# Kernel optimization log

Measured on AMD Instinct MI355X. Metric: run time of the kernel, lower is better.

The kernel has to match this reference:

```python
import jax, jax.numpy as jnp
import numpy as np

D = 1024
H = 16
HD = D // H
MLP = 4 * D
EPS = 1e-5


def layernorm(x, g, b):
    mu = jnp.mean(x, axis=-1, keepdims=True)
    var = jnp.mean(jnp.square(x - mu), axis=-1, keepdims=True)
    return (x - mu) * jax.lax.rsqrt(var + EPS) * g + b


def setup_inputs() -> dict:
    key = jax.random.key(0)
    ks = jax.random.split(key, 12)
    s = 0.02
    return {
        "x": jax.random.normal(ks[0], (2, 2048, D), jnp.float32),
        "ln1_g": jnp.ones((D,), jnp.float32),
        "ln1_b": jnp.zeros((D,), jnp.float32),
        "lnm_g": jnp.ones((D,), jnp.float32),
        "lnm_b": jnp.zeros((D,), jnp.float32),
        "qkv_w": jax.random.normal(ks[1], (D, 3 * D), jnp.float32) * s,
        "qkv_b": jnp.zeros((3 * D,), jnp.float32),
        "proj_w": jax.random.normal(ks[2], (D, D), jnp.float32) * s,
        "proj_b": jnp.zeros((D,), jnp.float32),
        "fc1_w": jax.random.normal(ks[3], (D, MLP), jnp.float32) * s,
        "fc1_b": jnp.zeros((MLP,), jnp.float32),
        "fc2_w": jax.random.normal(ks[4], (MLP, D), jnp.float32) * s,
        "fc2_b": jnp.zeros((D,), jnp.float32),
    }


def reference(x, ln1_g, ln1_b, lnm_g, lnm_b, qkv_w, qkv_b, proj_w, proj_b,
              fc1_w, fc1_b, fc2_w, fc2_b):
    B, N, _ = x.shape
    scale = HD ** -0.5
    # --- self-attention on norm1(x) ---
    h = layernorm(x, ln1_g, ln1_b)
    qkv = h @ qkv_w + qkv_b                       # [B, N, 3D]
    qkv = qkv.reshape(B, N, 3, H, HD)
    q, k, v = qkv[:, :, 0], qkv[:, :, 1], qkv[:, :, 2]  # [B, N, H, HD]
    attn = jnp.einsum("bqhd,bkhd->bhqk", q, k) * scale
    attn = jax.nn.softmax(attn, axis=-1)
    o = jnp.einsum("bhqk,bkhd->bqhd", attn, v).reshape(B, N, D)
    x = x + (o @ proj_w + proj_b)
    # --- MLP ---
    m = layernorm(x, lnm_g, lnm_b)
    m = jax.nn.gelu(m @ fc1_w + fc1_b, approximate=False)
    x = x + (m @ fc2_w + fc2_b)
    return x
```

## Files before the change

kernel.cpp:

```cpp
#include <hip/hip_runtime.h>

typedef __bf16 bf16_t;
typedef bf16_t bf16x4 __attribute__((ext_vector_type(4)));
typedef bf16_t bf16x8 __attribute__((ext_vector_type(8)));
typedef float f32x4 __attribute__((ext_vector_type(4)));
typedef unsigned short u16x8 __attribute__((ext_vector_type(8)));

#define MFMA(a, b, c) __builtin_amdgcn_mfma_f32_16x16x32_bf16(a, b, c, 0, 0, 0)

__device__ inline float exp2_fast(float x) {
  float r;
  asm volatile("v_exp_f32 %0, %1" : "=v"(r) : "v"(x));
  return r;
}

__device__ inline void gll16(const bf16_t* g, bf16_t* l) {
  __builtin_amdgcn_global_load_lds(
      (const __attribute__((address_space(1))) unsigned int*)(g),
      (__attribute__((address_space(3))) unsigned int*)(l), 16, 0, 0);
}

__device__ inline float gelu_f(float v) {
  float ax = fabsf(v) * 0.70710678118f;
  float t = __builtin_amdgcn_rcpf(1.0f + 0.3275911f * ax);
  float p = ((((1.061405429f * t - 1.453152027f) * t + 1.421413741f) * t -
              0.284496736f) * t + 0.254829592f) * t;
  float e = exp2_fast(-ax * ax * 1.4426950408889634f);
  float erf = 1.0f - p * e;
  erf = v < 0.f ? -erf : erf;
  return 0.5f * v * (1.0f + erf);
}

__global__ __launch_bounds__(256) void ln_kernel(const float* __restrict__ x,
                                                 const float* __restrict__ g,
                                                 const float* __restrict__ b,
                                                 bf16_t* __restrict__ out) {
  long row = blockIdx.x;
  const float4* xr = (const float4*)(x + row * 1024);
  float4 v = xr[threadIdx.x];
  float s = v.x + v.y + v.z + v.w;
  float s2 = v.x * v.x + v.y * v.y + v.z * v.z + v.w * v.w;
#pragma unroll
  for (int m = 32; m >= 1; m >>= 1) {
    s += __shfl_xor(s, m);
    s2 += __shfl_xor(s2, m);
  }
  __shared__ float red[8];
  int wid = threadIdx.x >> 6;
  if ((threadIdx.x & 63) == 0) {
    red[wid] = s;
    red[4 + wid] = s2;
  }
  __syncthreads();
  s = red[0] + red[1] + red[2] + red[3];
  s2 = red[4] + red[5] + red[6] + red[7];
  float mu = s * (1.f / 1024.f);
  float rs = rsqrtf(s2 * (1.f / 1024.f) - mu * mu + 1e-5f);
  float4 gv = ((const float4*)g)[threadIdx.x];
  float4 bv = ((const float4*)b)[threadIdx.x];
  bf16_t o0 = (bf16_t)((v.x - mu) * rs * gv.x + bv.x);
  bf16_t o1 = (bf16_t)((v.y - mu) * rs * gv.y + bv.y);
  bf16_t o2 = (bf16_t)((v.z - mu) * rs * gv.z + bv.z);
  bf16_t o3 = (bf16_t)((v.w - mu) * rs * gv.w + bv.w);
  ushort4 pk;
  pk.x = *(unsigned short*)&o0;
  pk.y = *(unsigned short*)&o1;
  pk.z = *(unsigned short*)&o2;
  pk.w = *(unsigned short*)&o3;
  *(ushort4*)(out + row * 1024 + threadIdx.x * 4) = pk;
}

__global__ __launch_bounds__(256) void wconv_all(
    const float* __restrict__ qkv_w, bf16_t* __restrict__ qkv_wt,
    const float* __restrict__ proj_w, bf16_t* __restrict__ proj_wt,
    const float* __restrict__ fc1_w, bf16_t* __restrict__ fc1_wt,
    const float* __restrict__ fc2_w, bf16_t* __restrict__ fc2_wt) {
  int id = blockIdx.x;
  const float* W;
  bf16_t* Wt;
  int K, N, bx, by;
  if (id < 768) {
    W = qkv_w; Wt = qkv_wt; K = 1024; N = 3072; bx = id % 48; by = id / 48;
  } else if (id < 1024) {
    int l = id - 768;
    W = proj_w; Wt = proj_wt; K = 1024; N = 1024; bx = l % 16; by = l / 16;
  } else if (id < 2048) {
    int l = id - 1024;
    W = fc1_w; Wt = fc1_wt; K = 1024; N = 4096; bx = l % 64; by = l / 64;
  } else {
    int l = id - 2048;
    W = fc2_w; Wt = fc2_wt; K = 4096; N = 1024; bx = l % 16; by = l / 16;
  }
  __shared__ float t[64][65];
  int n0 = bx * 64, k0 = by * 64;
  int tid = threadIdx.x;
  int c4 = tid & 15;
  int r = tid >> 4;
#pragma unroll
  for (int s = 0; s < 4; s++) {
    int k = r + s * 16;
    float4 v = *(const float4*)(W + (long)(k0 + k) * N + n0 + c4 * 4);
    t[k][c4 * 4] = v.x;
    t[k][c4 * 4 + 1] = v.y;
    t[k][c4 * 4 + 2] = v.z;
    t[k][c4 * 4 + 3] = v.w;
  }
  __syncthreads();
  int n = tid >> 2;
  int kc = (tid & 3) * 16;
  ushort4 pk[4];
#pragma unroll
  for (int c = 0; c < 4; c++) {
#pragma unroll
    for (int j = 0; j < 4; j++) {
      bf16_t x = (bf16_t)t[kc + c * 4 + j][n];
      ((unsigned short*)&pk[c])[j] = *(unsigned short*)&x;
    }
  }
  bf16_t* dst = Wt + (long)(n0 + n) * K + k0 + kc;
#pragma unroll
  for (int c = 0; c < 4; c++) *(ushort4*)(dst + c * 4) = pk[c];
}

#define STAGE_PTR(DA, DB, k0)                 \
  gll16(ga + (k0), DA + w * 512);             \
  gll16(ga + (k0) + astep, DA + 4096 + w * 512); \
  gll16(gb + (k0), DB + w * 512);

#define COMPUTE(LA, LB)                                                \
  {                                                                    \
    bf16x8 af[4], bfr[4];                                              \
    _Pragma("unroll") for (int mt = 0; mt < 4; mt++) af[mt] =          \
        *(const bf16x8*)(LA + (wm + mt * 16 + l15) * 32 + quad * 8);   \
    _Pragma("unroll") for (int nt = 0; nt < 4; nt++) bfr[nt] =         \
        *(const bf16x8*)(LB + (wn + nt * 16 + l15) * 32 + quad * 8);   \
    _Pragma("unroll") for (int mt = 0; mt < 4; mt++)                   \
        _Pragma("unroll") for (int nt = 0; nt < 4; nt++) acc[mt][nt] = \
            MFMA(af[mt], bfr[nt], acc[mt][nt]);                        \
  }

#define WB3 asm volatile("s_waitcnt vmcnt(3)\ns_barrier" ::: "memory")
#define WB0 asm volatile("s_waitcnt vmcnt(0)\ns_barrier" ::: "memory")

__global__ __launch_bounds__(512, 4) void gemm_kernel(
    const bf16_t* __restrict__ A, const bf16_t* __restrict__ Bt,
    const float* __restrict__ bias, const float* __restrict__ resid,
    void* __restrict__ Cout, int M, int N, int K, int epi) {
  __shared__ bf16_t lA0[256 * 32], lB0[128 * 32];
  __shared__ bf16_t lA1[256 * 32], lB1[128 * 32];
  __shared__ bf16_t lA2[256 * 32], lB2[128 * 32];
  int tid = threadIdx.x;
  int bn = blockIdx.x, bm = blockIdx.y;
  int kchunk = K / gridDim.z;
  int kbeg = blockIdx.z * kchunk, kend = kbeg + kchunk;

  int lane = tid & 63, w = tid >> 6;
  int quad = lane >> 4, l15 = lane & 15;
  int wm = (w & 3) * 64, wn = (w >> 2) * 64;

  f32x4 acc[4][4];
#pragma unroll
  for (int i = 0; i < 4; i++)
#pragma unroll
    for (int j = 0; j < 4; j++) acc[i][j] = (f32x4){0.f, 0.f, 0.f, 0.f};

  const bf16_t* ga = A + (long)(bm * 256 + w * 16 + (lane >> 2)) * K + (lane & 3) * 8;
  const bf16_t* gb = Bt + (long)(bn * 128 + w * 16 + (lane >> 2)) * K + (lane & 3) * 8;
  long astep = (long)128 * K;

  int nit = (kend - kbeg) >> 5;
  bf16_t *A0 = lA0, *A1 = lA1, *A2 = lA2;
  bf16_t *B0 = lB0, *B1 = lB1, *B2 = lB2;
  STAGE_PTR(A0, B0, kbeg);
  STAGE_PTR(A1, B1, kbeg + 32);
  for (int i = 0; i < nit; i++) {
    if (i + 1 < nit) { WB3; } else { WB0; }
    if (i + 2 < nit) {
      int ks = kbeg + (i + 2) * 32;
      STAGE_PTR(A2, B2, ks);
    }
    COMPUTE(A0, B0);
    bf16_t* t;
    t = A0; A0 = A1; A1 = A2; A2 = t;
    t = B0; B0 = B1; B1 = B2; B2 = t;
  }

#pragma unroll
  for (int mt = 0; mt < 4; mt++) {
#pragma unroll
    for (int r = 0; r < 4; r++) {
      long row = bm * 256 + wm + mt * 16 + quad * 4 + r;
#pragma unroll
      for (int nt = 0; nt < 4; nt++) {
        int col = bn * 128 + wn + nt * 16 + l15;
        long idx = row * N + col;
        if (epi == 3) {
          ((bf16_t*)Cout)[(long)blockIdx.z * M * N + idx] = (bf16_t)acc[mt][nt][r];
        } else {
          float v = acc[mt][nt][r] + bias[col];
          if (epi == 1) {
            ((float*)Cout)[idx] = v + resid[idx];
          } else if (epi == 2) {
            ((bf16_t*)Cout)[idx] = (bf16_t)gelu_f(v);
          } else {
            ((bf16_t*)Cout)[idx] = (bf16_t)v;
          }
        }
      }
    }
  }
}

__global__ __launch_bounds__(256) void reduce_ln_kernel(
    const bf16_t* __restrict__ p, const float* __restrict__ bias,
    const float* __restrict__ resid, float* __restrict__ x1,
    const float* __restrict__ g, const float* __restrict__ bb,
    bf16_t* __restrict__ mb) {
  const long MN = (long)4096 * 1024;
  long row = blockIdx.x;
  int t = threadIdx.x;
  bf16x4 a0 = *(const bf16x4*)(p + row * 1024 + t * 4);
  bf16x4 a1 = *(const bf16x4*)(p + MN + row * 1024 + t * 4);
  bf16x4 a2 = *(const bf16x4*)(p + 2 * MN + row * 1024 + t * 4);
  bf16x4 a3 = *(const bf16x4*)(p + 3 * MN + row * 1024 + t * 4);
  float4 r = ((const float4*)(resid + row * 1024))[t];
  float4 bv = ((const float4*)bias)[t];
  float4 v;
  v.x = (float)a0[0] + (float)a1[0] + (float)a2[0] + (float)a3[0] + r.x + bv.x;
  v.y = (float)a0[1] + (float)a1[1] + (float)a2[1] + (float)a3[1] + r.y + bv.y;
  v.z = (float)a0[2] + (float)a1[2] + (float)a2[2] + (float)a3[2] + r.z + bv.z;
  v.w = (float)a0[3] + (float)a1[3] + (float)a2[3] + (float)a3[3] + r.w + bv.w;
  ((float4*)(x1 + row * 1024))[t] = v;
  float s = v.x + v.y + v.z + v.w;
  float s2 = v.x * v.x + v.y * v.y + v.z * v.z + v.w * v.w;
#pragma unroll
  for (int m = 32; m >= 1; m >>= 1) {
    s += __shfl_xor(s, m);
    s2 += __shfl_xor(s2, m);
  }
  __shared__ float red[8];
  int wid = t >> 6;
  if ((t & 63) == 0) {
    red[wid] = s;
    red[4 + wid] = s2;
  }
  __syncthreads();
  s = red[0] + red[1] + red[2] + red[3];
  s2 = red[4] + red[5] + red[6] + red[7];
  float mu = s * (1.f / 1024.f);
  float rs = rsqrtf(s2 * (1.f / 1024.f) - mu * mu + 1e-5f);
  float4 gv = ((const float4*)g)[t];
  float4 b2 = ((const float4*)bb)[t];
  bf16_t o0 = (bf16_t)((v.x - mu) * rs * gv.x + b2.x);
  bf16_t o1 = (bf16_t)((v.y - mu) * rs * gv.y + b2.y);
  bf16_t o2 = (bf16_t)((v.z - mu) * rs * gv.z + b2.z);
  bf16_t o3 = (bf16_t)((v.w - mu) * rs * gv.w + b2.w);
  ushort4 pk;
  pk.x = *(unsigned short*)&o0;
  pk.y = *(unsigned short*)&o1;
  pk.z = *(unsigned short*)&o2;
  pk.w = *(unsigned short*)&o3;
  *(ushort4*)(mb + row * 1024 + t * 4) = pk;
}

__global__ __launch_bounds__(256) void reduce4_kernel(const bf16_t* __restrict__ p,
                                                      const float* __restrict__ bias,
                                                      const float* __restrict__ resid,
                                                      float* __restrict__ out) {
  long i = (long)blockIdx.x * 256 + threadIdx.x;
  const long MN = (long)4096 * 1024;
  bf16x4 a0 = *(const bf16x4*)(p + i * 4);
  bf16x4 a1 = *(const bf16x4*)(p + MN + i * 4);
  bf16x4 a2 = *(const bf16x4*)(p + 2 * MN + i * 4);
  bf16x4 a3 = *(const bf16x4*)(p + 3 * MN + i * 4);
  float4 r = ((const float4*)resid)[i];
  float4 bv = ((const float4*)bias)[i & 255];
  float4 o;
  o.x = (float)a0[0] + (float)a1[0] + (float)a2[0] + (float)a3[0] + r.x + bv.x;
  o.y = (float)a0[1] + (float)a1[1] + (float)a2[1] + (float)a3[1] + r.y + bv.y;
  o.z = (float)a0[2] + (float)a1[2] + (float)a2[2] + (float)a3[2] + r.z + bv.z;
  o.w = (float)a0[3] + (float)a1[3] + (float)a2[3] + (float)a3[3] + r.w + bv.w;
  ((float4*)out)[i] = o;
}

#define LDV 72

__global__ __launch_bounds__(256) void attn_kernel(const bf16_t* __restrict__ qkv,
                                                   bf16_t* __restrict__ o) {
  const int LD = 3072;
  int id = blockIdx.x;
  int within = id >> 3;
  int bh = (id & 7) * 4 + (within >> 4);
  int qt = within & 15;
  int h = bh & 15, b = bh >> 4;

  int tid = threadIdx.x, w = tid >> 6, lane = tid & 63;
  int quad = lane >> 4, l15 = lane & 15;
  int qrow = qt * 128 + w * 32;
  const bf16_t* base = qkv + (long)b * 2048 * LD + h * 64;
  const bf16_t* Qp = base;
  const bf16_t* Kp = base + 1024;
  const bf16_t* Vp = base + 2048;

  __shared__ bf16_t lK[2][64 * 64];
  __shared__ bf16_t lV[2][64 * LDV];
  __shared__ bf16_t lP[4][32 * LDV];
  bf16_t* myp = lP[w];

  const bf16_t* kg =
      Kp + (long)(w * 16 + (lane >> 3)) * LD + (((lane & 7) ^ (lane >> 3)) & 7) * 8;
  int kk = tid & 31;
  int d0 = (tid >> 5) * 8;
  const bf16_t* vg = Vp + (long)(2 * kk) * LD + d0;

  gll16(kg, lK[0] + w * 1024);
  gll16(kg + 8 * (long)LD, lK[0] + w * 1024 + 512);
  u16x8 va = *(const u16x8*)(vg);
  u16x8 vb = *(const u16x8*)(vg + LD);

  bf16x8 qf[2][2];
#pragma unroll
  for (int qi = 0; qi < 2; qi++)
#pragma unroll
    for (int d = 0; d < 2; d++)
      qf[qi][d] =
          *(const bf16x8*)(Qp + (long)(qrow + qi * 16 + l15) * LD + d * 32 + quad * 8);

  f32x4 oacc[2][4];
#pragma unroll
  for (int qi = 0; qi < 2; qi++)
#pragma unroll
    for (int t = 0; t < 4; t++) oacc[qi][t] = (f32x4){0.f, 0.f, 0.f, 0.f};
  float li_p[2][4] = {{0.f, 0.f, 0.f, 0.f}, {0.f, 0.f, 0.f, 0.f}};
  const float c2 = 0.18033688011112042f;

  int sw0 = (quad ^ l15) & 7;
  int sw1 = ((quad + 4) ^ l15) & 7;

  for (int it = 0; it < 32; it++) {
    int cur = it & 1, nxt = cur ^ 1;
    asm volatile("s_waitcnt vmcnt(0)\ns_barrier" ::: "memory");
    unsigned int* lvw = (unsigned int*)lV[cur];
#pragma unroll
    for (int j = 0; j < 8; j++)
      lvw[(d0 + j) * (LDV / 2) + kk] = (unsigned int)va[j] | ((unsigned int)vb[j] << 16);
    u16x8 va_n = va, vb_n = vb;
    if (it + 1 < 32) {
      long koff2 = (long)(it + 1) * 64 * LD;
      gll16(kg + koff2, lK[nxt] + w * 1024);
      gll16(kg + koff2 + 8 * (long)LD, lK[nxt] + w * 1024 + 512);
      va_n = *(const u16x8*)(vg + koff2);
      vb_n = *(const u16x8*)(vg + koff2 + LD);
    }
    asm volatile("s_waitcnt lgkmcnt(0)\ns_barrier" ::: "memory");

    bf16x8 kf[4][2];
#pragma unroll
    for (int st = 0; st < 4; st++) {
      const bf16_t* krow = lK[cur] + (st * 16 + l15) * 64;
      kf[st][0] = *(const bf16x8*)(krow + sw0 * 8);
      kf[st][1] = *(const bf16x8*)(krow + sw1 * 8);
    }
    f32x4 s[2][4];
#pragma unroll
    for (int qi = 0; qi < 2; qi++)
#pragma unroll
      for (int st = 0; st < 4; st++) {
        f32x4 z = (f32x4){0.f, 0.f, 0.f, 0.f};
        z = MFMA(qf[qi][0], kf[st][0], z);
        s[qi][st] = MFMA(qf[qi][1], kf[st][1], z);
      }

#pragma unroll
    for (int qi = 0; qi < 2; qi++)
#pragma unroll
      for (int st = 0; st < 4; st++)
#pragma unroll
        for (int r = 0; r < 4; r++) {
          float p = exp2_fast(s[qi][st][r] * c2);
          s[qi][st][r] = p;
          li_p[qi][r] += p;
        }

#pragma unroll
    for (int qi = 0; qi < 2; qi++)
#pragma unroll
      for (int r = 0; r < 4; r++)
#pragma unroll
        for (int st = 0; st < 4; st++)
          myp[(qi * 16 + quad * 4 + r) * LDV + st * 16 + l15] = (bf16_t)s[qi][st][r];
    asm volatile("s_waitcnt lgkmcnt(0)" ::: "memory");

    bf16x8 pa[2][2];
#pragma unroll
    for (int qi = 0; qi < 2; qi++) {
      pa[qi][0] = *(const bf16x8*)(myp + (qi * 16 + l15) * LDV + quad * 8);
      pa[qi][1] = *(const bf16x8*)(myp + (qi * 16 + l15) * LDV + 32 + quad * 8);
    }
#pragma unroll
    for (int t = 0; t < 4; t++) {
      const bf16_t* vr = lV[cur] + (t * 16 + l15) * LDV + quad * 8;
      bf16x8 v0 = *(const bf16x8*)(vr);
      bf16x8 v1 = *(const bf16x8*)(vr + 32);
#pragma unroll
      for (int qi = 0; qi < 2; qi++) {
        oacc[qi][t] = MFMA(pa[qi][0], v0, oacc[qi][t]);
        oacc[qi][t] = MFMA(pa[qi][1], v1, oacc[qi][t]);
      }
    }
    va = va_n;
    vb = vb_n;
  }

#pragma unroll
  for (int qi = 0; qi < 2; qi++) {
    float li[4];
#pragma unroll
    for (int r = 0; r < 4; r++) {
      float s = li_p[qi][r];
#pragma unroll
      for (int x = 8; x >= 1; x >>= 1) s += __shfl_xor(s, x);
      li[r] = s;
    }
#pragma unroll
    for (int t = 0; t < 4; t++)
#pragma unroll
      for (int r = 0; r < 4; r++) {
        long q = qrow + qi * 16 + quad * 4 + r;
        o[((long)b * 2048 + q) * 1024 + h * 64 + t * 16 + l15] =
            (bf16_t)(oacc[qi][t][r] / li[r]);
      }
  }
}

extern "C" void kernel_launch(void* const* d_in, const int* in_sizes, int n_in,
                              void* d_out, int out_size, void* d_ws, size_t ws_size,
                              hipStream_t stream) {
  (void)in_sizes; (void)n_in; (void)out_size; (void)ws_size;
  const float* x = (const float*)d_in[0];
  const float* ln1_g = (const float*)d_in[1];
  const float* ln1_b = (const float*)d_in[2];
  const float* lnm_g = (const float*)d_in[3];
  const float* lnm_b = (const float*)d_in[4];
  const float* qkv_w = (const float*)d_in[5];
  const float* qkv_b = (const float*)d_in[6];
  const float* proj_w = (const float*)d_in[7];
  const float* proj_b = (const float*)d_in[8];
  const float* fc1_w = (const float*)d_in[9];
  const float* fc1_b = (const float*)d_in[10];
  const float* fc2_w = (const float*)d_in[11];
  const float* fc2_b = (const float*)d_in[12];
  float* out = (float*)d_out;

  const int M = 4096;
  const int D_ = 1024, MLP_ = 4096, QKV = 3072;

  char* ws = (char*)d_ws;
  bf16_t* h = (bf16_t*)(ws);
  bf16_t* qkvb = (bf16_t*)(ws + (8u << 20));
  bf16_t* ob = (bf16_t*)(ws + (32u << 20));
  float* x1 = (float*)(ws + (40u << 20));
  bf16_t* mb = (bf16_t*)(ws + (56u << 20));
  bf16_t* gb = (bf16_t*)(ws + (64u << 20));
  bf16_t* qkv_wt = (bf16_t*)(ws + (96u << 20));
  bf16_t* proj_wt = (bf16_t*)(ws + (102u << 20));
  bf16_t* fc1_wt = (bf16_t*)(ws + (104u << 20));
  bf16_t* fc2_wt = (bf16_t*)(ws + (112u << 20));
  bf16_t* p_proj = (bf16_t*)(ws);
  bf16_t* p_fc2 = (bf16_t*)(ws);

  wconv_all<<<3072, 256, 0, stream>>>(qkv_w, qkv_wt, proj_w, proj_wt, fc1_w, fc1_wt,
                                      fc2_w, fc2_wt);

  ln_kernel<<<M, 256, 0, stream>>>(x, ln1_g, ln1_b, h);
  gemm_kernel<<<dim3(QKV / 128, M / 256), 512, 0, stream>>>(h, qkv_wt, qkv_b, nullptr,
                                                            qkvb, M, QKV, D_, 0);
  attn_kernel<<<512, 256, 0, stream>>>(qkvb, ob);
  gemm_kernel<<<dim3(D_ / 128, M / 256, 4), 512, 0, stream>>>(ob, proj_wt, nullptr,
                                                              nullptr, p_proj, M, D_,
                                                              D_, 3);
  reduce_ln_kernel<<<M, 256, 0, stream>>>(p_proj, proj_b, x, x1, lnm_g, lnm_b, mb);
  gemm_kernel<<<dim3(MLP_ / 128, M / 256), 512, 0, stream>>>(mb, fc1_wt, fc1_b,
                                                             nullptr, gb, M, MLP_, D_,
                                                             2);
  gemm_kernel<<<dim3(D_ / 128, M / 256, 4), 512, 0, stream>>>(gb, fc2_wt, nullptr,
                                                              nullptr, p_fc2, M, D_,
                                                              MLP_, 3);
  reduce4_kernel<<<4096, 256, 0, stream>>>(p_fc2, fc2_b, x1, out);
}
```

Baseline: 390.9 us.

## Add 256x256-tile triple-buffered GEMM for fc1 and fold softmax scale into Q

Adds a new GEMM kernel with 256x256 output tiles, 8 waves and a three-stage global-to-LDS pipeline, used only for the fc1+GELU GEMM. Larger tiles raise arithmetic intensity per loaded byte, but the grid shrinks to 256 blocks and register pressure goes up. Separately, the attention kernel pre-multiplies Q by the exp2 softmax scale once, removing a per-score multiply in the inner loop. That adds a bf16 rounding of the scaled Q values.

```diff
diff --git a/kernel.cpp b/kernel.cpp
--- a/kernel.cpp
+++ b/kernel.cpp
@@ -206,6 +206,82 @@
             ((bf16_t*)Cout)[idx] = (bf16_t)v;
           }
         }
+      }
+    }
+  }
+}
+
+#define STAGE256(DA, DB, k0)                  \
+  gll16(ga + (k0), DA + w * 512);             \
+  gll16(ga + (k0) + astep, DA + 4096 + w * 512); \
+  gll16(gb + (k0), DB + w * 512);             \
+  gll16(gb + (k0) + astep, DB + 4096 + w * 512);
+
+__global__ __launch_bounds__(512, 2) void gemm256_kernel(
+    const bf16_t* __restrict__ A, const bf16_t* __restrict__ Bt,
+    const float* __restrict__ bias, void* __restrict__ Cout, int M, int N, int K) {
+  __shared__ bf16_t lA0[256 * 32], lB0[256 * 32];
+  __shared__ bf16_t lA1[256 * 32], lB1[256 * 32];
+  __shared__ bf16_t lA2[256 * 32], lB2[256 * 32];
+  int tid = threadIdx.x;
+  int bn = blockIdx.x, bm = blockIdx.y;
+  int lane = tid & 63, w = tid >> 6;
+  int quad = lane >> 4, l15 = lane & 15;
+  int wm = (w & 3) * 64, wn = (w >> 2) * 128;
+
+  f32x4 acc[4][8];
+#pragma unroll
+  for (int i = 0; i < 4; i++)
+#pragma unroll
+    for (int j = 0; j < 8; j++) acc[i][j] = (f32x4){0.f, 0.f, 0.f, 0.f};
+
+  const bf16_t* ga = A + (long)(bm * 256 + w * 16 + (lane >> 2)) * K + (lane & 3) * 8;
+  const bf16_t* gb = Bt + (long)(bn * 256 + w * 16 + (lane >> 2)) * K + (lane & 3) * 8;
+  long astep = (long)128 * K;
+
+  int nit = K >> 5;
+  bf16_t *A0 = lA0, *A1 = lA1, *A2 = lA2;
+  bf16_t *B0 = lB0, *B1 = lB1, *B2 = lB2;
+  STAGE256(A0, B0, 0);
+  STAGE256(A1, B1, 32);
+  for (int i = 0; i < nit; i++) {
+    if (i + 1 < nit) {
+      asm volatile("s_waitcnt vmcnt(4)\ns_barrier" ::: "memory");
+    } else {
+      asm volatile("s_waitcnt vmcnt(0)\ns_barrier" ::: "memory");
+    }
+    if (i + 2 < nit) {
+      int ks = (i + 2) * 32;
+      STAGE256(A2, B2, ks);
+    }
+    {
+      bf16x8 af[4], bfr[8];
+#pragma unroll
+      for (int mt = 0; mt < 4; mt++)
+        af[mt] = *(const bf16x8*)(A0 + (wm + mt * 16 + l15) * 32 + quad * 8);
+#pragma unroll
+      for (int nt = 0; nt < 8; nt++)
+        bfr[nt] = *(const bf16x8*)(B0 + (wn + nt * 16 + l15) * 32 + quad * 8);
+#pragma unroll
+      for (int mt = 0; mt < 4; mt++)
+#pragma unroll
+        for (int nt = 0; nt < 8; nt++) acc[mt][nt] = MFMA(af[mt], bfr[nt], acc[mt][nt]);
+    }
+    bf16_t* t;
+    t = A0; A0 = A1; A1 = A2; A2 = t;
+    t = B0; B0 = B1; B1 = B2; B2 = t;
+  }
+
+#pragma unroll
+  for (int mt = 0; mt < 4; mt++) {
+#pragma unroll
+    for (int r = 0; r < 4; r++) {
+      long row = bm * 256 + wm + mt * 16 + quad * 4 + r;
+#pragma unroll
+      for (int nt = 0; nt < 8; nt++) {
+        int col = bn * 256 + wn + nt * 16 + l15;
+        float v = acc[mt][nt][r] + bias[col];
+        ((bf16_t*)Cout)[row * N + col] = (bf16_t)gelu_f(v);
       }
     }
   }
@@ -318,13 +394,17 @@
   u16x8 va = *(const u16x8*)(vg);
   u16x8 vb = *(const u16x8*)(vg + LD);
 
+  const float c2 = 0.18033688011112042f;
   bf16x8 qf[2][2];
 #pragma unroll
   for (int qi = 0; qi < 2; qi++)
 #pragma unroll
-    for (int d = 0; d < 2; d++)
-      qf[qi][d] =
+    for (int d = 0; d < 2; d++) {
+      bf16x8 q0 =
           *(const bf16x8*)(Qp + (long)(qrow + qi * 16 + l15) * LD + d * 32 + quad * 8);
+#pragma unroll
+      for (int j = 0; j < 8; j++) qf[qi][d][j] = (bf16_t)((float)q0[j] * c2);
+    }
 
   f32x4 oacc[2][4];
 #pragma unroll
@@ -332,7 +412,6 @@
 #pragma unroll
     for (int t = 0; t < 4; t++) oacc[qi][t] = (f32x4){0.f, 0.f, 0.f, 0.f};
   float li_p[2][4] = {{0.f, 0.f, 0.f, 0.f}, {0.f, 0.f, 0.f, 0.f}};
-  const float c2 = 0.18033688011112042f;
 
   int sw0 = (quad ^ l15) & 7;
   int sw1 = ((quad + 4) ^ l15) & 7;
@@ -377,7 +456,7 @@
       for (int st = 0; st < 4; st++)
 #pragma unroll
         for (int r = 0; r < 4; r++) {
-          float p = exp2_fast(s[qi][st][r] * c2);
+          float p = exp2_fast(s[qi][st][r]);
           s[qi][st][r] = p;
           li_p[qi][r] += p;
         }
@@ -480,9 +559,8 @@
                                                               nullptr, p_proj, M, D_,
                                                               D_, 3);
   reduce_ln_kernel<<<M, 256, 0, stream>>>(p_proj, proj_b, x, x1, lnm_g, lnm_b, mb);
-  gemm_kernel<<<dim3(MLP_ / 128, M / 256), 512, 0, stream>>>(mb, fc1_wt, fc1_b,
-                                                             nullptr, gb, M, MLP_, D_,
-                                                             2);
+  gemm256_kernel<<<dim3(MLP_ / 256, M / 256), 512, 0, stream>>>(mb, fc1_wt, fc1_b, gb,
+                                                                M, MLP_, D_);
   gemm_kernel<<<dim3(D_ / 128, M / 256, 4), 512, 0, stream>>>(gb, fc2_wt, nullptr,
                                                               nullptr, p_fc2, M, D_,
                                                               MLP_, 3);
```

Result: slower. 402.7 us (+3.0%).

## Split attention over two KV halves with merge kernel; fuse LN1 into weight conversion

Applied to the files above, without the earlier changes.

The attention kernel now splits the key/value sequence into two halves, doubling the grid to 1024 blocks. Each half writes unnormalized fp32 partial outputs and row sums, and a new merge kernel combines them into bf16. The softmax scale is folded into Q at load time, and the first layernorm moves into the weight-conversion launch to drop one kernel launch. The split aims to fill more CUs, at the cost of extra fp32 traffic (32MB partials written and read) and one more launch. Without a running max, merging the halves by summing exp values is only valid because the kernel already skips max subtraction.

```diff
diff --git a/kernel.cpp b/kernel.cpp
--- a/kernel.cpp
+++ b/kernel.cpp
@@ -31,51 +31,50 @@
   return 0.5f * v * (1.0f + erf);
 }
 
-__global__ __launch_bounds__(256) void ln_kernel(const float* __restrict__ x,
-                                                 const float* __restrict__ g,
-                                                 const float* __restrict__ b,
-                                                 bf16_t* __restrict__ out) {
-  long row = blockIdx.x;
-  const float4* xr = (const float4*)(x + row * 1024);
-  float4 v = xr[threadIdx.x];
-  float s = v.x + v.y + v.z + v.w;
-  float s2 = v.x * v.x + v.y * v.y + v.z * v.z + v.w * v.w;
-#pragma unroll
-  for (int m = 32; m >= 1; m >>= 1) {
-    s += __shfl_xor(s, m);
-    s2 += __shfl_xor(s2, m);
-  }
-  __shared__ float red[8];
-  int wid = threadIdx.x >> 6;
-  if ((threadIdx.x & 63) == 0) {
-    red[wid] = s;
-    red[4 + wid] = s2;
-  }
-  __syncthreads();
-  s = red[0] + red[1] + red[2] + red[3];
-  s2 = red[4] + red[5] + red[6] + red[7];
-  float mu = s * (1.f / 1024.f);
-  float rs = rsqrtf(s2 * (1.f / 1024.f) - mu * mu + 1e-5f);
-  float4 gv = ((const float4*)g)[threadIdx.x];
-  float4 bv = ((const float4*)b)[threadIdx.x];
-  bf16_t o0 = (bf16_t)((v.x - mu) * rs * gv.x + bv.x);
-  bf16_t o1 = (bf16_t)((v.y - mu) * rs * gv.y + bv.y);
-  bf16_t o2 = (bf16_t)((v.z - mu) * rs * gv.z + bv.z);
-  bf16_t o3 = (bf16_t)((v.w - mu) * rs * gv.w + bv.w);
-  ushort4 pk;
-  pk.x = *(unsigned short*)&o0;
-  pk.y = *(unsigned short*)&o1;
-  pk.z = *(unsigned short*)&o2;
-  pk.w = *(unsigned short*)&o3;
-  *(ushort4*)(out + row * 1024 + threadIdx.x * 4) = pk;
-}
-
 __global__ __launch_bounds__(256) void wconv_all(
     const float* __restrict__ qkv_w, bf16_t* __restrict__ qkv_wt,
     const float* __restrict__ proj_w, bf16_t* __restrict__ proj_wt,
     const float* __restrict__ fc1_w, bf16_t* __restrict__ fc1_wt,
-    const float* __restrict__ fc2_w, bf16_t* __restrict__ fc2_wt) {
+    const float* __restrict__ fc2_w, bf16_t* __restrict__ fc2_wt,
+    const float* __restrict__ x, const float* __restrict__ g1,
+    const float* __restrict__ b1, bf16_t* __restrict__ h) {
   int id = blockIdx.x;
+  if (id >= 3072) {
+    long row = id - 3072;
+    const float4* xr = (const float4*)(x + row * 1024);
+    float4 v = xr[threadIdx.x];
+    float s = v.x + v.y + v.z + v.w;
+    float s2 = v.x * v.x + v.y * v.y + v.z * v.z + v.w * v.w;
+#pragma unroll
+    for (int m = 32; m >= 1; m >>= 1) {
+      s += __shfl_xor(s, m);
+      s2 += __shfl_xor(s2, m);
+    }
+    __shared__ float red[8];
+    int wid = threadIdx.x >> 6;
+    if ((threadIdx.x & 63) == 0) {
+      red[wid] = s;
+      red[4 + wid] = s2;
+    }
+    __syncthreads();
+    s = red[0] + red[1] + red[2] + red[3];
+    s2 = red[4] + red[5] + red[6] + red[7];
+    float mu = s * (1.f / 1024.f);
+    float rs = rsqrtf(s2 * (1.f / 1024.f) - mu * mu + 1e-5f);
+    float4 gv = ((const float4*)g1)[threadIdx.x];
+    float4 bv = ((const float4*)b1)[threadIdx.x];
+    bf16_t o0 = (bf16_t)((v.x - mu) * rs * gv.x + bv.x);
+    bf16_t o1 = (bf16_t)((v.y - mu) * rs * gv.y + bv.y);
+    bf16_t o2 = (bf16_t)((v.z - mu) * rs * gv.z + bv.z);
+    bf16_t o3 = (bf16_t)((v.w - mu) * rs * gv.w + bv.w);
+    ushort4 pk;
+    pk.x = *(unsigned short*)&o0;
+    pk.y = *(unsigned short*)&o1;
+    pk.z = *(unsigned short*)&o2;
+    pk.w = *(unsigned short*)&o3;
+    *(ushort4*)(h + row * 1024 + threadIdx.x * 4) = pk;
+    return;
+  }
   const float* W;
   bf16_t* Wt;
   int K, N, bx, by;
@@ -113,8 +112,8 @@
   for (int c = 0; c < 4; c++) {
 #pragma unroll
     for (int j = 0; j < 4; j++) {
-      bf16_t x = (bf16_t)t[kc + c * 4 + j][n];
-      ((unsigned short*)&pk[c])[j] = *(unsigned short*)&x;
+      bf16_t xq = (bf16_t)t[kc + c * 4 + j][n];
+      ((unsigned short*)&pk[c])[j] = *(unsigned short*)&xq;
     }
   }
   bf16_t* dst = Wt + (long)(n0 + n) * K + k0 + kc;
@@ -286,12 +285,15 @@
 #define LDV 72
 
 __global__ __launch_bounds__(256) void attn_kernel(const bf16_t* __restrict__ qkv,
-                                                   bf16_t* __restrict__ o) {
+                                                   float* __restrict__ oa,
+                                                   float* __restrict__ li_g) {
   const int LD = 3072;
   int id = blockIdx.x;
   int within = id >> 3;
-  int bh = (id & 7) * 4 + (within >> 4);
-  int qt = within & 15;
+  int bh = (id & 7) * 4 + (within >> 5);
+  int local = within & 31;
+  int qt = local >> 1;
+  int ks = local & 1;
   int h = bh & 15, b = bh >> 4;
 
   int tid = threadIdx.x, w = tid >> 6, lane = tid & 63;
@@ -299,8 +301,8 @@
   int qrow = qt * 128 + w * 32;
   const bf16_t* base = qkv + (long)b * 2048 * LD + h * 64;
   const bf16_t* Qp = base;
-  const bf16_t* Kp = base + 1024;
-  const bf16_t* Vp = base + 2048;
+  const bf16_t* Kp = base + 1024 + (long)ks * 1024 * LD;
+  const bf16_t* Vp = base + 2048 + (long)ks * 1024 * LD;
 
   __shared__ bf16_t lK[2][64 * 64];
   __shared__ bf16_t lV[2][64 * LDV];
@@ -318,13 +320,17 @@
   u16x8 va = *(const u16x8*)(vg);
   u16x8 vb = *(const u16x8*)(vg + LD);
 
+  const float c2 = 0.18033688011112042f;
   bf16x8 qf[2][2];
 #pragma unroll
   for (int qi = 0; qi < 2; qi++)
 #pragma unroll
-    for (int d = 0; d < 2; d++)
-      qf[qi][d] =
+    for (int d = 0; d < 2; d++) {
+      bf16x8 q0 =
           *(const bf16x8*)(Qp + (long)(qrow + qi * 16 + l15) * LD + d * 32 + quad * 8);
+#pragma unroll
+      for (int j = 0; j < 8; j++) qf[qi][d][j] = (bf16_t)((float)q0[j] * c2);
+    }
 
   f32x4 oacc[2][4];
 #pragma unroll
@@ -332,12 +338,11 @@
 #pragma unroll
     for (int t = 0; t < 4; t++) oacc[qi][t] = (f32x4){0.f, 0.f, 0.f, 0.f};
   float li_p[2][4] = {{0.f, 0.f, 0.f, 0.f}, {0.f, 0.f, 0.f, 0.f}};
-  const float c2 = 0.18033688011112042f;
 
   int sw0 = (quad ^ l15) & 7;
   int sw1 = ((quad + 4) ^ l15) & 7;
 
-  for (int it = 0; it < 32; it++) {
+  for (int it = 0; it < 16; it++) {
     int cur = it & 1, nxt = cur ^ 1;
     asm volatile("s_waitcnt vmcnt(0)\ns_barrier" ::: "memory");
     unsigned int* lvw = (unsigned int*)lV[cur];
@@ -345,7 +350,7 @@
     for (int j = 0; j < 8; j++)
       lvw[(d0 + j) * (LDV / 2) + kk] = (unsigned int)va[j] | ((unsigned int)vb[j] << 16);
     u16x8 va_n = va, vb_n = vb;
-    if (it + 1 < 32) {
+    if (it + 1 < 16) {
       long koff2 = (long)(it + 1) * 64 * LD;
       gll16(kg + koff2, lK[nxt] + w * 1024);
       gll16(kg + koff2 + 8 * (long)LD, lK[nxt] + w * 1024 + 512);
@@ -377,7 +382,7 @@
       for (int st = 0; st < 4; st++)
 #pragma unroll
         for (int r = 0; r < 4; r++) {
-          float p = exp2_fast(s[qi][st][r] * c2);
+          float p = exp2_fast(s[qi][st][r]);
           s[qi][st][r] = p;
           li_p[qi][r] += p;
         }
@@ -412,6 +417,7 @@
     vb = vb_n;
   }
 
+  float* oap = oa + (long)ks * 4096 * 1024;
 #pragma unroll
   for (int qi = 0; qi < 2; qi++) {
     float li[4];
@@ -422,15 +428,45 @@
       for (int x = 8; x >= 1; x >>= 1) s += __shfl_xor(s, x);
       li[r] = s;
     }
+    if (l15 == 0) {
+      long q = qrow + qi * 16 + quad * 4;
+      float4 lv = {li[0], li[1], li[2], li[3]};
+      *(float4*)(li_g + ((long)ks * 32 + b * 16 + h) * 2048 + q) = lv;
+    }
 #pragma unroll
     for (int t = 0; t < 4; t++)
 #pragma unroll
       for (int r = 0; r < 4; r++) {
         long q = qrow + qi * 16 + quad * 4 + r;
-        o[((long)b * 2048 + q) * 1024 + h * 64 + t * 16 + l15] =
-            (bf16_t)(oacc[qi][t][r] / li[r]);
+        oap[((long)b * 2048 + q) * 1024 + h * 64 + t * 16 + l15] = oacc[qi][t][r];
       }
   }
+}
+
+__global__ __launch_bounds__(256) void attn_merge(const float* __restrict__ oa,
+                                                  const float* __restrict__ li_g,
+                                                  bf16_t* __restrict__ ob) {
+  const long MN = (long)4096 * 1024;
+  long row = blockIdx.x;
+  int t = threadIdx.x;
+  int b = (int)(row >> 11);
+  int q = (int)(row & 2047);
+  int h = (t * 4) >> 6;
+  float l0 = li_g[((long)b * 16 + h) * 2048 + q];
+  float l1 = li_g[((long)32 + b * 16 + h) * 2048 + q];
+  float inv = 1.0f / (l0 + l1);
+  float4 a = ((const float4*)(oa + row * 1024))[t];
+  float4 c = ((const float4*)(oa + MN + row * 1024))[t];
+  bf16_t o0 = (bf16_t)((a.x + c.x) * inv);
+  bf16_t o1 = (bf16_t)((a.y + c.y) * inv);
+  bf16_t o2 = (bf16_t)((a.z + c.z) * inv);
+  bf16_t o3 = (bf16_t)((a.w + c.w) * inv);
+  ushort4 pk;
+  pk.x = *(unsigned short*)&o0;
+  pk.y = *(unsigned short*)&o1;
+  pk.z = *(unsigned short*)&o2;
+  pk.w = *(unsigned short*)&o3;
+  *(ushort4*)(ob + row * 1024 + t * 4) = pk;
 }
 
 extern "C" void kernel_launch(void* const* d_in, const int* in_sizes, int n_in,
@@ -460,7 +496,9 @@
   bf16_t* qkvb = (bf16_t*)(ws + (8u << 20));
   bf16_t* ob = (bf16_t*)(ws + (32u << 20));
   float* x1 = (float*)(ws + (40u << 20));
-  bf16_t* mb = (bf16_t*)(ws + (56u << 20));
+  float* li_g = (float*)(ws + (56u << 20));
+  bf16_t* mb = (bf16_t*)(ws + (57u << 20));
+  float* oa = (float*)(ws + (64u << 20));
   bf16_t* gb = (bf16_t*)(ws + (64u << 20));
   bf16_t* qkv_wt = (bf16_t*)(ws + (96u << 20));
   bf16_t* proj_wt = (bf16_t*)(ws + (102u << 20));
@@ -468,14 +506,14 @@
   bf16_t* fc2_wt = (bf16_t*)(ws + (112u << 20));
   bf16_t* p_proj = (bf16_t*)(ws);
   bf16_t* p_fc2 = (bf16_t*)(ws);
-
-  wconv_all<<<3072, 256, 0, stream>>>(qkv_w, qkv_wt, proj_w, proj_wt, fc1_w, fc1_wt,
-                                      fc2_w, fc2_wt);
-
-  ln_kernel<<<M, 256, 0, stream>>>(x, ln1_g, ln1_b, h);
+  mb = (bf16_t*)(ws + (120u << 20));
+
+  wconv_all<<<7168, 256, 0, stream>>>(qkv_w, qkv_wt, proj_w, proj_wt, fc1_w, fc1_wt,
+                                      fc2_w, fc2_wt, x, ln1_g, ln1_b, h);
   gemm_kernel<<<dim3(QKV / 128, M / 256), 512, 0, stream>>>(h, qkv_wt, qkv_b, nullptr,
                                                             qkvb, M, QKV, D_, 0);
-  attn_kernel<<<512, 256, 0, stream>>>(qkvb, ob);
+  attn_kernel<<<1024, 256, 0, stream>>>(qkvb, oa, li_g);
+  attn_merge<<<4096, 256, 0, stream>>>(oa, li_g, ob);
   gemm_kernel<<<dim3(D_ / 128, M / 256, 4), 512, 0, stream>>>(ob, proj_wt, nullptr,
                                                               nullptr, p_proj, M, D_,
                                                               D_, 3);
```

After: 390.9 us. No clear change (+0.0%).
